# Optimization experiments

Measured on AMD Instinct MI355X. Metric: run time of the kernel, lower is better.

## Reference

```python
import jax, jax.numpy as jnp
import numpy as np

B = 8192          # batch of agents
K = 4             # max_neighbors
NUM_LANES = 12
LANE_F = 4        # obs_dim // num_lanes = 48 // 12
HEADS = 4
OUT = 32          # gat_output_dim per head
EMB = HEADS * OUT # 128, gat_per_lane_output / intersection emb dim
HID = 64          # graphsage_hidden_dim
GRU_H = 32        # gru_hidden_dim
ALPHA = 0.2       # leaky relu slope

# Lane cooperation: lanes of the same approach (4 approaches x 3 lanes) cooperate.
_blk = np.kron(np.eye(4), np.ones((3, 3))).astype(np.float32)
LANE_COOP = jnp.asarray(_blk)
LANE_CONF = jnp.asarray(1.0 - _blk)


def _gat_stream(x, W, a_src, a_dst, adj):
    # x: [N, 12, 4]; W: [H, 4, O]; a_*: [H, O]; adj: [12, 12]
    Wh = jnp.einsum('nlf,hfo->nhlo', x, W)                      # [N,H,12,O]
    e_s = jnp.einsum('nhlo,ho->nhl', Wh, a_src)
    e_d = jnp.einsum('nhlo,ho->nhl', Wh, a_dst)
    e = jax.nn.leaky_relu(e_s[..., :, None] + e_d[..., None, :], ALPHA)  # [N,H,12,12]
    e = jnp.where(adj[None, None] > 0, e, jnp.float32(-1e9))
    att = jax.nn.softmax(e, axis=-1)
    out = jnp.einsum('nhij,nhjo->niho', att, Wh)                # [N,12,H,O]
    return jax.nn.elu(out.reshape(out.shape[0], NUM_LANES, EMB))


def _gru_final(xs, Wih, Whh, bih, bhh):
    # xs: [K, B, HID] -> final hidden [B, GRU_H], torch GRU gate convention (r,z,n)
    def step(h, x):
        gi = x @ Wih + bih
        gh = h @ Whh + bhh
        i_r, i_z, i_n = jnp.split(gi, 3, axis=-1)
        h_r, h_z, h_n = jnp.split(gh, 3, axis=-1)
        r = jax.nn.sigmoid(i_r + h_r)
        z = jax.nn.sigmoid(i_z + h_z)
        n = jnp.tanh(i_n + r * h_n)
        return (1.0 - z) * n + z * h, None
    h0 = jnp.zeros((xs.shape[1], Whh.shape[0]), xs.dtype)
    hT, _ = jax.lax.scan(step, h0, xs)
    return hT


def setup_inputs() -> dict:
    key = jax.random.key(0)
    ks = jax.random.split(key, 24)
    rn = lambda k, s: (jax.random.normal(k, s, jnp.float32) * 0.1)
    z = lambda n: jnp.zeros((n,), jnp.float32)
    return {
        'self_features': jax.random.normal(ks[0], (B, 48), jnp.float32),
        'neighbor_features': jax.random.normal(ks[1], (B, K, 48), jnp.float32),
        'neighbor_mask': (jax.random.uniform(ks[2], (B, K)) > 0.25).astype(jnp.float32),
        'neighbor_directions': jax.random.randint(ks[3], (B, K), 0, 4).astype(jnp.float32) * 0.25,
        # dual-stream GAT params
        'W_coop': rn(ks[4], (HEADS, LANE_F, OUT)), 'a_src_coop': rn(ks[5], (HEADS, OUT)), 'a_dst_coop': rn(ks[6], (HEADS, OUT)),
        'W_conf': rn(ks[7], (HEADS, LANE_F, OUT)), 'a_src_conf': rn(ks[8], (HEADS, OUT)), 'a_dst_conf': rn(ks[9], (HEADS, OUT)),
        'W_fuse': rn(ks[10], (2 * EMB, EMB)), 'b_fuse': z(EMB),
        # GraphSAGE neighbor projection (+1 for direction feature)
        'W_proj': rn(ks[11], (EMB + 1, HID)), 'b_proj': z(HID),
        # BiGRU (fwd/bwd), torch layout transposed: Wih [HID,3H], Whh [H,3H]
        'Wih_f': rn(ks[12], (HID, 3 * GRU_H)), 'Whh_f': rn(ks[13], (GRU_H, 3 * GRU_H)), 'bih_f': z(3 * GRU_H), 'bhh_f': z(3 * GRU_H),
        'Wih_b': rn(ks[14], (HID, 3 * GRU_H)), 'Whh_b': rn(ks[15], (GRU_H, 3 * GRU_H)), 'bih_b': z(3 * GRU_H), 'bhh_b': z(3 * GRU_H),
        # combine self + BiGRU summary -> network embedding
        'W_out': rn(ks[16], (EMB + 2 * GRU_H, HID)), 'b_out': z(HID),
    }


def reference(self_features, neighbor_features, neighbor_mask, neighbor_directions,
              W_coop, a_src_coop, a_dst_coop, W_conf, a_src_conf, a_dst_conf,
              W_fuse, b_fuse, W_proj, b_proj,
              Wih_f, Whh_f, bih_f, bhh_f, Wih_b, Whh_b, bih_b, bhh_b,
              W_out, b_out):
    Bc, Kc = neighbor_features.shape[:2]
    # run dual-stream GAT on self + all neighbors in one batch of small lane graphs
    allx = jnp.concatenate([self_features[:, None, :], neighbor_features], axis=1)
    allx = allx.reshape(Bc * (Kc + 1), NUM_LANES, LANE_F)
    coop = _gat_stream(allx, W_coop, a_src_coop, a_dst_coop, LANE_COOP)
    conf = _gat_stream(allx, W_conf, a_src_conf, a_dst_conf, LANE_CONF)
    fused = jax.nn.elu(jnp.concatenate([coop, conf], axis=-1) @ W_fuse + b_fuse)  # [N,12,128]
    emb = fused.mean(axis=1).reshape(Bc, Kc + 1, EMB)  # mean pool over lanes
    self_emb = emb[:, 0]          # [B,128]
    nbr_emb = emb[:, 1:]          # [B,K,128]
    # GraphSAGE projection of neighbors (direction-aware), masked
    nbr_in = jnp.concatenate([nbr_emb, neighbor_directions[..., None]], axis=-1)
    x = jax.nn.relu(nbr_in @ W_proj + b_proj) * neighbor_mask[..., None]  # [B,K,HID]
    xs = jnp.swapaxes(x, 0, 1)    # [K,B,HID]
    h_f = _gru_final(xs, Wih_f, Whh_f, bih_f, bhh_f)
    h_b = _gru_final(xs[::-1], Wih_b, Whh_b, bih_b, bhh_b)
    net = jax.nn.relu(jnp.concatenate([self_emb, h_f, h_b], axis=-1) @ W_out + b_out)  # [B,64]
    return jnp.concatenate([self_emb, net], axis=-1)  # [B,192]
```

## Files before the change

kernel.cpp:

```cpp
#include <hip/hip_runtime.h>
#include <hip/hip_bf16.h>
#include <math.h>

typedef short short8 __attribute__((ext_vector_type(8)));
typedef float f32x4  __attribute__((ext_vector_type(4)));

__device__ __forceinline__ unsigned short f2b(float f) {
  union { float f; unsigned int u; } x; x.f = f;
  return (unsigned short)((x.u + 0x7FFFu + ((x.u >> 16) & 1u)) >> 16);
}
__device__ __forceinline__ float b2f_u(unsigned short u) {
  union { unsigned int u; float f; } x; x.u = ((unsigned int)u) << 16;
  return x.f;
}
__device__ __forceinline__ unsigned int pkbf(float a, float b) {
  union { __hip_bfloat162 h; unsigned int u; } c;
  c.h = __float22bfloat162_rn(make_float2(a, b));
  return c.u;
}
__device__ __forceinline__ float sigm(float x) {
  return __builtin_amdgcn_rcpf(1.f + __expf(-x));
}
__device__ __forceinline__ float tanhfast(float x) {
  float ax = fabsf(x);
  float em = __expf(-2.f * ax);
  float t  = (1.f - em) * __builtin_amdgcn_rcpf(1.f + em);
  return copysignf(t, x);
}
__device__ __forceinline__ float eluf(float v) {
  return v > 0.f ? v : (__expf(v) - 1.f);
}

__global__ __launch_bounds__(256) void prepack_kernel(
    const float* __restrict__ Wf,
    const float* __restrict__ Wc, const float* __restrict__ Wn,
    const float* __restrict__ as_c, const float* __restrict__ ad_c,
    const float* __restrict__ as_n, const float* __restrict__ ad_n,
    const float* __restrict__ Wproj,
    const float* __restrict__ Wih_f, const float* __restrict__ Wih_b,
    const float* __restrict__ Wout,
    const float* __restrict__ Whh_f, const float* __restrict__ Whh_b,
    unsigned short* __restrict__ fragB,
    unsigned short* __restrict__ fragWB,
    float* __restrict__ Wa,
    unsigned short* __restrict__ fragP,
    unsigned short* __restrict__ fragIH,
    unsigned short* __restrict__ fragO,
    unsigned short* __restrict__ fragHH)
{
  int e = blockIdx.x * 256 + threadIdx.x;
  unsigned short tmp[8];
  if (e < 4096) {
    int kb = e >> 9, tile = (e >> 6) & 7, lane = e & 63;
    int n = tile * 16 + (lane & 15);
    int kbase = kb * 32 + (lane >> 4) * 8;
#pragma unroll
    for (int j = 0; j < 8; j++) tmp[j] = f2b(Wf[(kbase + j) * 128 + n]);
    *(short8*)(fragB + e * 8) = *(short8*)tmp;
  } else if (e < 5120) {
    int i = e - 4096;
    int s = i >> 9, tile = (i >> 6) & 7, lane = i & 63;
    int c15 = lane & 15, quad = lane >> 4;
    int n = tile * 16 + c15;
    int h = n >> 5, o = n & 31;
    const float* W = s ? Wn : Wc;
#pragma unroll
    for (int j = 0; j < 8; j++) {
      int k = quad * 8 + j;
      tmp[j] = ((k >> 2) == h) ? f2b(W[h * 128 + (k & 3) * 32 + o])
                               : (unsigned short)0;
    }
    *(short8*)(fragWB + i * 8) = *(short8*)tmp;
  } else if (e < 5184) {
    int i = e - 5120;
    int s = i >> 5, d = (i >> 4) & 1, h = (i >> 2) & 3, f = i & 3;
    const float* W = s ? Wn : Wc;
    const float* a = s ? (d ? ad_n : as_n) : (d ? ad_c : as_c);
    float acc = 0.f;
#pragma unroll
    for (int o = 0; o < 32; o++) acc += W[h * 128 + f * 32 + o] * a[h * 32 + o];
    Wa[i] = acc;
  } else if (e < 6208) {
    int i = e - 5184;
    int kb = i >> 8, nt = (i >> 6) & 3, lane = i & 63;
    int c15 = lane & 15, quad = lane >> 4;
#pragma unroll
    for (int j = 0; j < 8; j++)
      tmp[j] = f2b(Wproj[(kb * 32 + quad * 8 + j) * 64 + nt * 16 + c15]);
    *(short8*)(fragP + i * 8) = *(short8*)tmp;
  } else if (e < 7744) {
    int i = e - 6208;
    int d = (i >= 768), r = i - d * 768;
    int kb = r / 384, nt = (r >> 6) % 6, lane = r & 63;
    int c15 = lane & 15, quad = lane >> 4;
    const float* W = d ? Wih_b : Wih_f;
#pragma unroll
    for (int j = 0; j < 8; j++)
      tmp[j] = f2b(W[(kb * 32 + quad * 8 + j) * 96 + nt * 16 + c15]);
    *(short8*)(fragIH + i * 8) = *(short8*)tmp;
  } else if (e < 9280) {
    int r = e - 7744;
    int kb = r >> 8, nt = (r >> 6) & 3, lane = r & 63;
    int c15 = lane & 15, quad = lane >> 4;
#pragma unroll
    for (int j = 0; j < 8; j++)
      tmp[j] = f2b(Wout[(kb * 32 + quad * 8 + j) * 64 + nt * 16 + c15]);
    *(short8*)(fragO + r * 8) = *(short8*)tmp;
  } else if (e < 10048) {
    int i = e - 9280;
    int d = i / 384, r = i - d * 384;
    int nt = r >> 6, lane = r & 63;
    int c15 = lane & 15, quad = lane >> 4;
    const float* W = d ? Whh_b : Whh_f;
#pragma unroll
    for (int j = 0; j < 8; j++)
      tmp[j] = f2b(W[(quad * 8 + j) * 96 + nt * 16 + c15]);
    *(short8*)(fragHH + i * 8) = *(short8*)tmp;
  }
}

__global__ __launch_bounds__(256) void gat_fuse_kernel(
    const float* __restrict__ self_f, const float* __restrict__ nbr_f,
    const float* __restrict__ Wa,
    const unsigned short* __restrict__ fragWB,
    const unsigned short* __restrict__ fragB,
    const float* __restrict__ b_fuse,
    unsigned short* __restrict__ embb,
    float* __restrict__ out,
    int npairs)
{
  const int tid = threadIdx.x;
  const int w = tid >> 6, lane = tid & 63, c15 = lane & 15, quad = lane >> 4;

  __shared__ __align__(16) float sxf[2][12][4];
  __shared__ __align__(16) float sWa[64];
  __shared__ float sed[2][2][4][12];
  __shared__ __align__(16) unsigned short sA[2][2][16][24];
  __shared__ __align__(16) unsigned short scatb[2][16][268];
  __shared__ __align__(16) float sbias[128];

  if (tid < 32) ((f32x4*)sbias)[tid] = ((const f32x4*)b_fuse)[tid];
  else if (tid < 48) ((f32x4*)sWa)[tid - 32] = ((const f32x4*)Wa)[tid - 32];
  if (tid >= 128) {
    int t = tid - 128;
    int g = t >> 6, s = (t >> 5) & 1, i = 12 + ((t >> 3) & 3), cp = t & 7;
    *(unsigned int*)&sA[g][s][i][cp * 2] = 0u;
  }

  const int g_q = w & 1, s_q = w >> 1;
  const unsigned short* __restrict__ pwb3 = fragWB + (s_q * 8 * 64 + lane) * 8;
  const unsigned short* __restrict__ pwb4 = fragB + (2 * w * 64 + lane) * 8;

  const int start = blockIdx.x * 4;
  const int end   = min(npairs, start + 4);

  f32x4 xr = {0.f, 0.f, 0.f, 0.f};
  int xnd = 0, xq = 0;
  if (tid < 24) {
    xnd = (tid >= 12); xq = tid - xnd * 12;
    int nn = start * 2 + xnd, b = nn / 5, slot = nn - b * 5;
    const float* src = slot ? (nbr_f + (b * 4 + slot - 1) * 48)
                            : (self_f + b * 48);
    xr = *(const f32x4*)(src + xq * 4);
  }

  for (int it = start; it < end; ++it) {
    const int n0 = it * 2;
    if (tid < 24) ((f32x4*)&sxf[xnd][0][0])[xq] = xr;
    __syncthreads();
    if (tid < 24 && it + 1 < end) {
      int nn = (it + 1) * 2 + xnd, b = nn / 5, slot = nn - b * 5;
      const float* src = slot ? (nbr_f + (b * 4 + slot - 1) * 48)
                              : (self_f + b * 48);
      xr = *(const f32x4*)(src + xq * 4);
    }

    if (lane < 48) {
      int h = lane / 12, i = lane - h * 12;
      f32x4 xv  = *(const f32x4*)&sxf[g_q][i][0];
      f32x4 was = *(const f32x4*)&sWa[s_q * 32 + h * 4];
      f32x4 wad = *(const f32x4*)&sWa[s_q * 32 + 16 + h * 4];
      float es = xv[0]*was[0] + xv[1]*was[1] + xv[2]*was[2] + xv[3]*was[3];
      float ed = xv[0]*wad[0] + xv[1]*wad[1] + xv[2]*wad[2] + xv[3]*wad[3];
      sed[g_q][s_q][h][i] = ed;
      int blk3 = (i / 3) * 3;
      float xa0 = 0.f, xa1 = 0.f, xa2 = 0.f, xa3 = 0.f, sum = 0.f;
      if (s_q == 0) {
#pragma unroll
        for (int jj = 0; jj < 3; jj++) {
          int j = blk3 + jj;
          float e = es + sed[g_q][0][h][j];
          e = e > 0.f ? e : 0.2f * e;
          float p = __expf(e);
          sum += p;
          f32x4 xj = *(const f32x4*)&sxf[g_q][j][0];
          xa0 += p * xj[0]; xa1 += p * xj[1];
          xa2 += p * xj[2]; xa3 += p * xj[3];
        }
      } else {
#pragma unroll
        for (int jj = 0; jj < 9; jj++) {
          int j = jj < blk3 ? jj : jj + 3;
          float e = es + sed[g_q][1][h][j];
          e = e > 0.f ? e : 0.2f * e;
          float p = __expf(e);
          sum += p;
          f32x4 xj = *(const f32x4*)&sxf[g_q][j][0];
          xa0 += p * xj[0]; xa1 += p * xj[1];
          xa2 += p * xj[2]; xa3 += p * xj[3];
        }
      }
      float inv = 1.f / sum;
      uint2 pk = make_uint2(pkbf(xa0 * inv, xa1 * inv),
                            pkbf(xa2 * inv, xa3 * inv));
      *(uint2*)&sA[g_q][s_q][i][h * 4] = pk;
    }

    {
      const short8 z8 = {0,0,0,0,0,0,0,0};
      short8 xb = z8;
      if (quad < 2) xb = *(const short8*)&sA[g_q][s_q][c15][quad * 8];
#pragma unroll
      for (int tile = 0; tile < 8; tile++) {
        short8 aw = *(const short8*)(pwb3 + tile * 512);
        f32x4 c = {0.f, 0.f, 0.f, 0.f};
        c = __builtin_amdgcn_mfma_f32_16x16x32_bf16(aw, xb, c, 0, 0, 0);
        uint2 pk = make_uint2(pkbf(eluf(c[0]), eluf(c[1])),
                              pkbf(eluf(c[2]), eluf(c[3])));
        *(uint2*)&scatb[g_q][c15][s_q * 128 + tile * 16 + (quad << 2)] = pk;
      }
    }
    __syncthreads();

    {
      f32x4 acc[2][2];
#pragma unroll
      for (int nd = 0; nd < 2; nd++)
#pragma unroll
        for (int tt = 0; tt < 2; tt++) acc[nd][tt] = (f32x4){0.f,0.f,0.f,0.f};
#pragma unroll
      for (int kb = 0; kb < 8; kb++) {
        short8 a0 = *(const short8*)&scatb[0][c15][kb * 32 + (quad << 3)];
        short8 a1 = *(const short8*)&scatb[1][c15][kb * 32 + (quad << 3)];
#pragma unroll
        for (int tt = 0; tt < 2; tt++) {
          short8 bw = *(const short8*)(pwb4 + kb * 4096 + tt * 512);
          acc[0][tt] = __builtin_amdgcn_mfma_f32_16x16x32_bf16(a0, bw, acc[0][tt], 0, 0, 0);
          acc[1][tt] = __builtin_amdgcn_mfma_f32_16x16x32_bf16(a1, bw, acc[1][tt], 0, 0, 0);
        }
      }
      float tot[2][2];
#pragma unroll
      for (int nd = 0; nd < 2; nd++) {
#pragma unroll
        for (int tt = 0; tt < 2; tt++) {
          float p = 0.f;
          if (quad < 3) {
            float bcol = sbias[w * 32 + tt * 16 + c15];
#pragma unroll
            for (int r = 0; r < 4; r++) p += eluf(acc[nd][tt][r] + bcol);
          }
          p += __shfl_xor(p, 16);
          p += __shfl_xor(p, 32);
          tot[nd][tt] = p;
        }
      }
      int ndw = quad >> 1, ttw = quad & 1;
      float val = (ndw ? (ttw ? tot[1][1] : tot[1][0])
                       : (ttw ? tot[0][1] : tot[0][0])) * (1.f / 12.f);
      int node = n0 + ndw;
      int col  = w * 32 + ttw * 16 + c15;
      embb[node * 128 + col] = f2b(val);
      int bq = node / 5;
      if (node == bq * 5) out[bq * 192 + col] = val;
    }
  }
}

__global__ __launch_bounds__(256) void head_kernel(
    const unsigned short* __restrict__ embb,
    const float* __restrict__ maskp, const float* __restrict__ dirsp,
    const float* __restrict__ W_proj, const float* __restrict__ b_proj,
    const unsigned short* __restrict__ fragP,
    const unsigned short* __restrict__ fragIH,
    const unsigned short* __restrict__ fragHH,
    const float* __restrict__ bih_f, const float* __restrict__ bhh_f,
    const float* __restrict__ bih_b, const float* __restrict__ bhh_b,
    const unsigned short* __restrict__ fragO,
    const float* __restrict__ b_out,
    float* __restrict__ out)
{
  const int b8 = blockIdx.x * 8;
  const int tid = threadIdx.x;
  const int w = tid >> 6, lane = tid & 63, c15 = lane & 15, quad = lane >> 4;

  __shared__ __align__(16) unsigned short sX[32][72];
  __shared__ __align__(16) unsigned short sgi[2][32][96];
  __shared__ float sH[2][8][32];
  __shared__ __align__(16) unsigned short sHb[2][16][32];
  __shared__ __align__(16) float sgh[2][8][96];
  __shared__ __align__(16) unsigned short sCat[16][200];
  __shared__ __align__(16) float sPB[128];
  __shared__ __align__(16) float sBI[2][96], sBH[2][96];
  __shared__ __align__(16) float sBO[64];

  if (tid < 64) { sPB[tid] = b_proj[tid]; sPB[64 + tid] = W_proj[128 * 64 + tid]; sBO[tid] = b_out[tid]; }
  if (tid < 96) { sBI[0][tid] = bih_f[tid]; sBI[1][tid] = bih_b[tid];
                  sBH[0][tid] = bhh_f[tid]; sBH[1][tid] = bhh_b[tid]; }
  {
    unsigned int* hb = (unsigned int*)sHb;
    hb[tid] = 0u; hb[tid + 256] = 0u;
    float* hz = (float*)sH;
    for (int i = tid; i < 512; i += 256) hz[i] = 0.f;
  }
  __syncthreads();

  {
    const int mt  = w >> 1;
    const int nt0 = (w & 1) * 2;
    const int sloc = mt * 4 + (c15 >> 2);
    const int nbr  = c15 & 3;
    const unsigned short* brow = embb + (((b8 + sloc) * 5) + 1 + nbr) * 128;
    short8 xb[4];
#pragma unroll
    for (int kb = 0; kb < 4; kb++)
      xb[kb] = *(const short8*)(brow + kb * 32 + quad * 8);
    f32x4 acc0 = {0.f,0.f,0.f,0.f}, acc1 = acc0;
#pragma unroll
    for (int kb = 0; kb < 4; kb++) {
      short8 a0 = *(const short8*)(fragP + ((kb * 4 + nt0    ) * 64 + lane) * 8);
      short8 a1 = *(const short8*)(fragP + ((kb * 4 + nt0 + 1) * 64 + lane) * 8);
      acc0 = __builtin_amdgcn_mfma_f32_16x16x32_bf16(a0, xb[kb], acc0, 0, 0, 0);
      acc1 = __builtin_amdgcn_mfma_f32_16x16x32_bf16(a1, xb[kb], acc1, 0, 0, 0);
    }
    const float dirv  = dirsp[(b8 + sloc) * 4 + nbr];
    const float maskv = maskp[(b8 + sloc) * 4 + nbr];
#pragma unroll
    for (int tt = 0; tt < 2; tt++) {
      f32x4 c = tt ? acc1 : acc0;
      int colb = (nt0 + tt) * 16 + (quad << 2);
      f32x4 wp = *(const f32x4*)&sPB[64 + colb];
      f32x4 pb = *(const f32x4*)&sPB[colb];
      float v0 = fmaxf(c[0] + dirv * wp[0] + pb[0], 0.f) * maskv;
      float v1 = fmaxf(c[1] + dirv * wp[1] + pb[1], 0.f) * maskv;
      float v2 = fmaxf(c[2] + dirv * wp[2] + pb[2], 0.f) * maskv;
      float v3 = fmaxf(c[3] + dirv * wp[3] + pb[3], 0.f) * maskv;
      uint2 pk = make_uint2(pkbf(v0, v1), pkbf(v2, v3));
      *(uint2*)&sX[mt * 16 + c15][colb] = pk;
    }
  }
  __syncthreads();

  {
    const int mt  = w >> 1;
    const int ntb = (w & 1) * 3;
    short8 xb0 = *(const short8*)&sX[mt * 16 + c15][quad * 8];
    short8 xb1 = *(const short8*)&sX[mt * 16 + c15][32 + quad * 8];
#pragma unroll
    for (int d = 0; d < 2; d++) {
#pragma unroll
      for (int t2 = 0; t2 < 3; t2++) {
        int nt = ntb + t2;
        f32x4 acc = {0.f,0.f,0.f,0.f};
        short8 a0 = *(const short8*)(fragIH + ((d * 12 +     nt) * 64 + lane) * 8);
        short8 a1 = *(const short8*)(fragIH + ((d * 12 + 6 + nt) * 64 + lane) * 8);
        acc = __builtin_amdgcn_mfma_f32_16x16x32_bf16(a0, xb0, acc, 0, 0, 0);
        acc = __builtin_amdgcn_mfma_f32_16x16x32_bf16(a1, xb1, acc, 0, 0, 0);
        f32x4 bi = *(const f32x4*)&sBI[d][nt * 16 + (quad << 2)];
        uint2 pk = make_uint2(pkbf(acc[0] + bi[0], acc[1] + bi[1]),
                              pkbf(acc[2] + bi[2], acc[3] + bi[3]));
        *(uint2*)&sgi[d][mt * 16 + c15][nt * 16 + (quad << 2)] = pk;
      }
    }
    if (tid >= 128) {
      int t = tid - 128;
      int s = t >> 4, c8 = (t & 15) * 8;
      short8 v = *(const short8*)(embb + (b8 + s) * 5 * 128 + c8);
      *(short8*)&sCat[s][c8] = v;
    }
  }
  __syncthreads();

  {
    const int d = w >> 1;
    const int q = w & 1;
    const int u = lane & 31, sp = lane >> 5;
    for (int step = 0; step < 4; step++) {
      short8 hb = *(const short8*)&sHb[d][c15][quad * 8];
#pragma unroll
      for (int nt = 0; nt < 6; nt++) {
        short8 aw = *(const short8*)(fragHH + ((d * 6 + nt) * 64 + lane) * 8);
        f32x4 c = {0.f,0.f,0.f,0.f};
        c = __builtin_amdgcn_mfma_f32_16x16x32_bf16(aw, hb, c, 0, 0, 0);
        if ((c15 >> 2) == q)
          *(f32x4*)&sgh[d][c15][nt * 16 + (quad << 2)] = c;
      }
      const int k = d ? (3 - step) : step;
#pragma unroll
      for (int si = 0; si < 2; si++) {
        int s = q * 4 + sp + si * 2;
        int row = s * 4 + k;
        float ghr = sgh[d][s][u]      + sBH[d][u];
        float ghz = sgh[d][s][32 + u] + sBH[d][32 + u];
        float ghn = sgh[d][s][64 + u] + sBH[d][64 + u];
        float r = sigm(b2f_u(sgi[d][row][u]) + ghr);
        float z = sigm(b2f_u(sgi[d][row][32 + u]) + ghz);
        float n = tanhfast(b2f_u(sgi[d][row][64 + u]) + r * ghn);
        float h = (1.f - z) * n + z * sH[d][s][u];
        sH[d][s][u] = h;
        sHb[d][s][u] = f2b(h);
        if (step == 3) sCat[s][128 + d * 32 + u] = f2b(h);
      }
    }
  }
  __syncthreads();

  {
    const int nt = w;
    f32x4 acc = {0.f,0.f,0.f,0.f};
#pragma unroll
    for (int kb = 0; kb < 6; kb++) {
      short8 bb = *(const short8*)&sCat[c15][kb * 32 + quad * 8];
      short8 aw = *(const short8*)(fragO + ((kb * 4 + nt) * 64 + lane) * 8);
      acc = __builtin_amdgcn_mfma_f32_16x16x32_bf16(aw, bb, acc, 0, 0, 0);
    }
    if (c15 < 8) {
      f32x4 bo = *(const f32x4*)&sBO[nt * 16 + (quad << 2)];
      f32x4 v;
      v[0] = fmaxf(acc[0] + bo[0], 0.f);
      v[1] = fmaxf(acc[1] + bo[1], 0.f);
      v[2] = fmaxf(acc[2] + bo[2], 0.f);
      v[3] = fmaxf(acc[3] + bo[3], 0.f);
      *(f32x4*)(out + (b8 + c15) * 192 + 128 + nt * 16 + (quad << 2)) = v;
    }
  }
}

extern "C" void kernel_launch(void* const* d_in, const int* in_sizes, int n_in,
                              void* d_out, int out_size, void* d_ws, size_t ws_size,
                              hipStream_t stream) {
  const float* self_f  = (const float*)d_in[0];
  const float* nbr_f   = (const float*)d_in[1];
  const float* maskp   = (const float*)d_in[2];
  const float* dirsp   = (const float*)d_in[3];
  const float* W_coop  = (const float*)d_in[4];
  const float* as_coop = (const float*)d_in[5];
  const float* ad_coop = (const float*)d_in[6];
  const float* W_conf  = (const float*)d_in[7];
  const float* as_conf = (const float*)d_in[8];
  const float* ad_conf = (const float*)d_in[9];
  const float* W_fuse  = (const float*)d_in[10];
  const float* b_fuse  = (const float*)d_in[11];
  const float* W_proj  = (const float*)d_in[12];
  const float* b_proj  = (const float*)d_in[13];
  const float* Wih_f   = (const float*)d_in[14];
  const float* Whh_f   = (const float*)d_in[15];
  const float* bih_f   = (const float*)d_in[16];
  const float* bhh_f   = (const float*)d_in[17];
  const float* Wih_b   = (const float*)d_in[18];
  const float* Whh_b   = (const float*)d_in[19];
  const float* bih_b   = (const float*)d_in[20];
  const float* bhh_b   = (const float*)d_in[21];
  const float* W_out   = (const float*)d_in[22];
  const float* b_out   = (const float*)d_in[23];

  const int B = in_sizes[0] / 48;
  char* ws = (char*)d_ws;
  unsigned short* fragB  = (unsigned short*)(ws);
  unsigned short* fragWB = (unsigned short*)(ws + 65536);
  float*          Wa     = (float*)(ws + 81920);
  unsigned short* fragP  = (unsigned short*)(ws + 82176);
  unsigned short* fragIH = (unsigned short*)(ws + 98560);
  unsigned short* fragO  = (unsigned short*)(ws + 123136);
  unsigned short* fragHH = (unsigned short*)(ws + 147712);
  unsigned short* embb   = (unsigned short*)(ws + 160000);

  prepack_kernel<<<40, 256, 0, stream>>>(
      W_fuse, W_coop, W_conf, as_coop, ad_coop, as_conf, ad_conf,
      W_proj, Wih_f, Wih_b, W_out, Whh_f, Whh_b,
      fragB, fragWB, Wa, fragP, fragIH, fragO, fragHH);

  const int npairs = B * 5 / 2;
  gat_fuse_kernel<<<npairs / 4, 256, 0, stream>>>(
      self_f, nbr_f, Wa, fragWB, fragB, b_fuse, embb, (float*)d_out, npairs);

  head_kernel<<<B / 8, 256, 0, stream>>>(
      embb, maskp, dirsp, W_proj, b_proj, fragP, fragIH, fragHH,
      bih_f, bhh_f, bih_b, bhh_b,
      fragO, b_out, (float*)d_out);
}
```

Before: 242.4 us.

## Process two node pairs per 512-thread block without a serial loop

The GAT+fuse kernel now uses 512-thread blocks that each handle 4 nodes (two pairs) in a single pass, where before each 256-thread block looped over 4 pairs with a software prefetch. Bias and attention weights are loaded straight into registers rather than staged in shared memory. The aim is to remove the per-iteration loop and its barriers and expose more parallelism through more waves in flight. In exchange it drops the prefetch overlap, launches more blocks, and uses more shared memory per block.

```diff
diff --git a/kernel.cpp b/kernel.cpp
--- a/kernel.cpp
+++ b/kernel.cpp
@@ -119,7 +119,7 @@
   }
 }
 
-__global__ __launch_bounds__(256) void gat_fuse_kernel(
+__global__ __launch_bounds__(512) void gat_fuse_kernel(
     const float* __restrict__ self_f, const float* __restrict__ nbr_f,
     const float* __restrict__ Wa,
     const unsigned short* __restrict__ fragWB,
@@ -131,149 +131,139 @@
 {
   const int tid = threadIdx.x;
   const int w = tid >> 6, lane = tid & 63, c15 = lane & 15, quad = lane >> 4;
-
-  __shared__ __align__(16) float sxf[2][12][4];
-  __shared__ __align__(16) float sWa[64];
-  __shared__ float sed[2][2][4][12];
-  __shared__ __align__(16) unsigned short sA[2][2][16][24];
-  __shared__ __align__(16) unsigned short scatb[2][16][268];
-  __shared__ __align__(16) float sbias[128];
-
-  if (tid < 32) ((f32x4*)sbias)[tid] = ((const f32x4*)b_fuse)[tid];
-  else if (tid < 48) ((f32x4*)sWa)[tid - 32] = ((const f32x4*)Wa)[tid - 32];
-  if (tid >= 128) {
-    int t = tid - 128;
-    int g = t >> 6, s = (t >> 5) & 1, i = 12 + ((t >> 3) & 3), cp = t & 7;
-    *(unsigned int*)&sA[g][s][i][cp * 2] = 0u;
-  }
-
-  const int g_q = w & 1, s_q = w >> 1;
-  const unsigned short* __restrict__ pwb3 = fragWB + (s_q * 8 * 64 + lane) * 8;
-  const unsigned short* __restrict__ pwb4 = fragB + (2 * w * 64 + lane) * 8;
-
-  const int start = blockIdx.x * 4;
-  const int end   = min(npairs, start + 4);
-
-  f32x4 xr = {0.f, 0.f, 0.f, 0.f};
-  int xnd = 0, xq = 0;
-  if (tid < 24) {
-    xnd = (tid >= 12); xq = tid - xnd * 12;
-    int nn = start * 2 + xnd, b = nn / 5, slot = nn - b * 5;
+  const int pr = w >> 2;
+  const int wq = w & 3;
+  const int g_q = wq & 1, s_q = wq >> 1;
+  const int ng  = pr * 2 + g_q;
+  const int n0  = blockIdx.x * 4 + pr * 2;
+
+  __shared__ __align__(16) float sxf[4][12][4];
+  __shared__ float sed[4][2][4][12];
+  __shared__ __align__(16) unsigned short sA[4][2][16][24];
+  __shared__ __align__(16) unsigned short scatb[4][16][268];
+
+  if (tid < 384) {
+    int g4 = tid / 96, r = tid - g4 * 96;
+    int s = r / 48, rr = r - s * 48;
+    int row = 12 + rr / 12, cp = rr % 12;
+    *(unsigned int*)&sA[g4][s][row][cp * 2] = 0u;
+  }
+  if (tid < 48) {
+    int nd4 = tid / 12, q = tid - nd4 * 12;
+    int nn = blockIdx.x * 4 + nd4, b = nn / 5, slot = nn - b * 5;
     const float* src = slot ? (nbr_f + (b * 4 + slot - 1) * 48)
                             : (self_f + b * 48);
-    xr = *(const f32x4*)(src + xq * 4);
-  }
-
-  for (int it = start; it < end; ++it) {
-    const int n0 = it * 2;
-    if (tid < 24) ((f32x4*)&sxf[xnd][0][0])[xq] = xr;
-    __syncthreads();
-    if (tid < 24 && it + 1 < end) {
-      int nn = (it + 1) * 2 + xnd, b = nn / 5, slot = nn - b * 5;
-      const float* src = slot ? (nbr_f + (b * 4 + slot - 1) * 48)
-                              : (self_f + b * 48);
-      xr = *(const f32x4*)(src + xq * 4);
-    }
-
-    if (lane < 48) {
-      int h = lane / 12, i = lane - h * 12;
-      f32x4 xv  = *(const f32x4*)&sxf[g_q][i][0];
-      f32x4 was = *(const f32x4*)&sWa[s_q * 32 + h * 4];
-      f32x4 wad = *(const f32x4*)&sWa[s_q * 32 + 16 + h * 4];
-      float es = xv[0]*was[0] + xv[1]*was[1] + xv[2]*was[2] + xv[3]*was[3];
-      float ed = xv[0]*wad[0] + xv[1]*wad[1] + xv[2]*wad[2] + xv[3]*wad[3];
-      sed[g_q][s_q][h][i] = ed;
-      int blk3 = (i / 3) * 3;
-      float xa0 = 0.f, xa1 = 0.f, xa2 = 0.f, xa3 = 0.f, sum = 0.f;
-      if (s_q == 0) {
-#pragma unroll
-        for (int jj = 0; jj < 3; jj++) {
-          int j = blk3 + jj;
-          float e = es + sed[g_q][0][h][j];
-          e = e > 0.f ? e : 0.2f * e;
-          float p = __expf(e);
-          sum += p;
-          f32x4 xj = *(const f32x4*)&sxf[g_q][j][0];
-          xa0 += p * xj[0]; xa1 += p * xj[1];
-          xa2 += p * xj[2]; xa3 += p * xj[3];
+    ((f32x4*)&sxf[nd4][0][0])[q] = *(const f32x4*)(src + q * 4);
+  }
+  f32x4 was, wad;
+  {
+    int hh = lane < 48 ? (lane / 12) : 3;
+    was = *(const f32x4*)(Wa + s_q * 32 + hh * 4);
+    wad = *(const f32x4*)(Wa + s_q * 32 + 16 + hh * 4);
+  }
+  const float bias0 = b_fuse[wq * 32 + c15];
+  const float bias1 = b_fuse[wq * 32 + 16 + c15];
+  const unsigned short* __restrict__ pwb3 = fragWB + (s_q * 8 * 64 + lane) * 8;
+  const unsigned short* __restrict__ pwb4 = fragB + (2 * wq * 64 + lane) * 8;
+
+  __syncthreads();
+
+  if (lane < 48) {
+    int h = lane / 12, i = lane - h * 12;
+    f32x4 xv = *(const f32x4*)&sxf[ng][i][0];
+    float es = xv[0]*was[0] + xv[1]*was[1] + xv[2]*was[2] + xv[3]*was[3];
+    float ed = xv[0]*wad[0] + xv[1]*wad[1] + xv[2]*wad[2] + xv[3]*wad[3];
+    sed[ng][s_q][h][i] = ed;
+    int blk3 = (i / 3) * 3;
+    float xa0 = 0.f, xa1 = 0.f, xa2 = 0.f, xa3 = 0.f, sum = 0.f;
+    if (s_q == 0) {
+#pragma unroll
+      for (int jj = 0; jj < 3; jj++) {
+        int j = blk3 + jj;
+        float e = es + sed[ng][0][h][j];
+        e = e > 0.f ? e : 0.2f * e;
+        float p = __expf(e);
+        sum += p;
+        f32x4 xj = *(const f32x4*)&sxf[ng][j][0];
+        xa0 += p * xj[0]; xa1 += p * xj[1];
+        xa2 += p * xj[2]; xa3 += p * xj[3];
+      }
+    } else {
+#pragma unroll
+      for (int jj = 0; jj < 9; jj++) {
+        int j = jj < blk3 ? jj : jj + 3;
+        float e = es + sed[ng][1][h][j];
+        e = e > 0.f ? e : 0.2f * e;
+        float p = __expf(e);
+        sum += p;
+        f32x4 xj = *(const f32x4*)&sxf[ng][j][0];
+        xa0 += p * xj[0]; xa1 += p * xj[1];
+        xa2 += p * xj[2]; xa3 += p * xj[3];
+      }
+    }
+    float inv = 1.f / sum;
+    uint2 pk = make_uint2(pkbf(xa0 * inv, xa1 * inv),
+                          pkbf(xa2 * inv, xa3 * inv));
+    *(uint2*)&sA[ng][s_q][i][h * 4] = pk;
+  }
+
+  {
+    const short8 z8 = {0,0,0,0,0,0,0,0};
+    short8 xb = z8;
+    if (quad < 2) xb = *(const short8*)&sA[ng][s_q][c15][quad * 8];
+#pragma unroll
+    for (int tile = 0; tile < 8; tile++) {
+      short8 aw = *(const short8*)(pwb3 + tile * 512);
+      f32x4 c = {0.f, 0.f, 0.f, 0.f};
+      c = __builtin_amdgcn_mfma_f32_16x16x32_bf16(aw, xb, c, 0, 0, 0);
+      uint2 pk = make_uint2(pkbf(eluf(c[0]), eluf(c[1])),
+                            pkbf(eluf(c[2]), eluf(c[3])));
+      *(uint2*)&scatb[ng][c15][s_q * 128 + tile * 16 + (quad << 2)] = pk;
+    }
+  }
+  __syncthreads();
+
+  {
+    f32x4 acc[2][2];
+#pragma unroll
+    for (int nd = 0; nd < 2; nd++)
+#pragma unroll
+      for (int tt = 0; tt < 2; tt++) acc[nd][tt] = (f32x4){0.f,0.f,0.f,0.f};
+#pragma unroll
+    for (int kb = 0; kb < 8; kb++) {
+      short8 a0 = *(const short8*)&scatb[pr * 2 + 0][c15][kb * 32 + (quad << 3)];
+      short8 a1 = *(const short8*)&scatb[pr * 2 + 1][c15][kb * 32 + (quad << 3)];
+#pragma unroll
+      for (int tt = 0; tt < 2; tt++) {
+        short8 bw = *(const short8*)(pwb4 + kb * 4096 + tt * 512);
+        acc[0][tt] = __builtin_amdgcn_mfma_f32_16x16x32_bf16(a0, bw, acc[0][tt], 0, 0, 0);
+        acc[1][tt] = __builtin_amdgcn_mfma_f32_16x16x32_bf16(a1, bw, acc[1][tt], 0, 0, 0);
+      }
+    }
+    float tot[2][2];
+#pragma unroll
+    for (int nd = 0; nd < 2; nd++) {
+#pragma unroll
+      for (int tt = 0; tt < 2; tt++) {
+        float p = 0.f;
+        if (quad < 3) {
+          float bcol = tt ? bias1 : bias0;
+#pragma unroll
+          for (int r = 0; r < 4; r++) p += eluf(acc[nd][tt][r] + bcol);
         }
-      } else {
-#pragma unroll
-        for (int jj = 0; jj < 9; jj++) {
-          int j = jj < blk3 ? jj : jj + 3;
-          float e = es + sed[g_q][1][h][j];
-          e = e > 0.f ? e : 0.2f * e;
-          float p = __expf(e);
-          sum += p;
-          f32x4 xj = *(const f32x4*)&sxf[g_q][j][0];
-          xa0 += p * xj[0]; xa1 += p * xj[1];
-          xa2 += p * xj[2]; xa3 += p * xj[3];
-        }
-      }
-      float inv = 1.f / sum;
-      uint2 pk = make_uint2(pkbf(xa0 * inv, xa1 * inv),
-                            pkbf(xa2 * inv, xa3 * inv));
-      *(uint2*)&sA[g_q][s_q][i][h * 4] = pk;
-    }
-
-    {
-      const short8 z8 = {0,0,0,0,0,0,0,0};
-      short8 xb = z8;
-      if (quad < 2) xb = *(const short8*)&sA[g_q][s_q][c15][quad * 8];
-#pragma unroll
-      for (int tile = 0; tile < 8; tile++) {
-        short8 aw = *(const short8*)(pwb3 + tile * 512);
-        f32x4 c = {0.f, 0.f, 0.f, 0.f};
-        c = __builtin_amdgcn_mfma_f32_16x16x32_bf16(aw, xb, c, 0, 0, 0);
-        uint2 pk = make_uint2(pkbf(eluf(c[0]), eluf(c[1])),
-                              pkbf(eluf(c[2]), eluf(c[3])));
-        *(uint2*)&scatb[g_q][c15][s_q * 128 + tile * 16 + (quad << 2)] = pk;
-      }
-    }
-    __syncthreads();
-
-    {
-      f32x4 acc[2][2];
-#pragma unroll
-      for (int nd = 0; nd < 2; nd++)
-#pragma unroll
-        for (int tt = 0; tt < 2; tt++) acc[nd][tt] = (f32x4){0.f,0.f,0.f,0.f};
-#pragma unroll
-      for (int kb = 0; kb < 8; kb++) {
-        short8 a0 = *(const short8*)&scatb[0][c15][kb * 32 + (quad << 3)];
-        short8 a1 = *(const short8*)&scatb[1][c15][kb * 32 + (quad << 3)];
-#pragma unroll
-        for (int tt = 0; tt < 2; tt++) {
-          short8 bw = *(const short8*)(pwb4 + kb * 4096 + tt * 512);
-          acc[0][tt] = __builtin_amdgcn_mfma_f32_16x16x32_bf16(a0, bw, acc[0][tt], 0, 0, 0);
-          acc[1][tt] = __builtin_amdgcn_mfma_f32_16x16x32_bf16(a1, bw, acc[1][tt], 0, 0, 0);
-        }
-      }
-      float tot[2][2];
-#pragma unroll
-      for (int nd = 0; nd < 2; nd++) {
-#pragma unroll
-        for (int tt = 0; tt < 2; tt++) {
-          float p = 0.f;
-          if (quad < 3) {
-            float bcol = sbias[w * 32 + tt * 16 + c15];
-#pragma unroll
-            for (int r = 0; r < 4; r++) p += eluf(acc[nd][tt][r] + bcol);
-          }
-          p += __shfl_xor(p, 16);
-          p += __shfl_xor(p, 32);
-          tot[nd][tt] = p;
-        }
-      }
-      int ndw = quad >> 1, ttw = quad & 1;
-      float val = (ndw ? (ttw ? tot[1][1] : tot[1][0])
-                       : (ttw ? tot[0][1] : tot[0][0])) * (1.f / 12.f);
-      int node = n0 + ndw;
-      int col  = w * 32 + ttw * 16 + c15;
-      embb[node * 128 + col] = f2b(val);
-      int bq = node / 5;
-      if (node == bq * 5) out[bq * 192 + col] = val;
-    }
+        p += __shfl_xor(p, 16);
+        p += __shfl_xor(p, 32);
+        tot[nd][tt] = p;
+      }
+    }
+    int ndw = quad >> 1, ttw = quad & 1;
+    float val = (ndw ? (ttw ? tot[1][1] : tot[1][0])
+                     : (ttw ? tot[0][1] : tot[0][0])) * (1.f / 12.f);
+    int node = n0 + ndw;
+    int col  = wq * 32 + ttw * 16 + c15;
+    embb[node * 128 + col] = f2b(val);
+    int bq = node / 5;
+    if (node == bq * 5) out[bq * 192 + col] = val;
   }
 }
 
@@ -481,7 +471,7 @@
       fragB, fragWB, Wa, fragP, fragIH, fragO, fragHH);
 
   const int npairs = B * 5 / 2;
-  gat_fuse_kernel<<<npairs / 4, 256, 0, stream>>>(
+  gat_fuse_kernel<<<npairs / 2, 512, 0, stream>>>(
       self_f, nbr_f, Wa, fragWB, fragB, b_fuse, embb, (float*)d_out, npairs);
 
   head_kernel<<<B / 8, 256, 0, stream>>>(
```

After: 224.7 us. 7.3% less time.
